# Kernel optimization log

Hardware: AMD Instinct MI355X
Metric: run time of the kernel (lower is better)

## Reference

```python
import jax, jax.numpy as jnp
import numpy as np


def setup_inputs() -> dict:
    key = jax.random.key(0)
    k_x, k_m, k_w1, k_b1, k_w2, k_b2 = jax.random.split(key, 6)
    b, seq_len, d_in, d_out = 8, 4096, 1024, 512
    x = jax.random.normal(k_x, (b, seq_len, d_in), dtype=jnp.float32)
    # binary-ish mask in {0,1} as floats (torch code multiplies by mask)
    mask = (jax.random.uniform(k_m, (b, seq_len)) < 0.5).astype(jnp.float32)
    s1 = 1.0 / np.sqrt(d_in)
    s2 = 1.0 / np.sqrt(d_out)
    W_enc = jax.random.uniform(k_w1, (d_out, d_in), minval=-s1, maxval=s1, dtype=jnp.float32)
    b_enc = jax.random.uniform(k_b1, (d_out,), minval=-s1, maxval=s1, dtype=jnp.float32)
    W_dec = jax.random.uniform(k_w2, (d_in, d_out), minval=-s2, maxval=s2, dtype=jnp.float32)
    b_dec = jax.random.uniform(k_b2, (d_in,), minval=-s2, maxval=s2, dtype=jnp.float32)
    return {"x": x, "mask": mask, "W_enc": W_enc, "b_enc": b_enc, "W_dec": W_dec, "b_dec": b_dec}


def reference(x, mask, W_enc, b_enc, W_dec, b_dec):
    # per-step: v_t = v_{t-1} + relu(x_t @ W_enc^T + b_enc) * mask_t  -> additive scan == cumsum
    h = jax.nn.relu(jnp.einsum('bsd,od->bso', x, W_enc) + b_enc) * mask[:, :, None]  # [b,s,d_out]
    v_cum = jnp.cumsum(h, axis=1)  # [b,s,d_out]
    out_enc = jnp.einsum('bso,do->bsd', v_cum, W_dec) + b_dec  # decode every prefix state
    v = v_cum[:, -1, :]  # final accumulated state
    return (v, out_enc)
```

## Files before the change

kernel.cpp:

```cpp
#include <hip/hip_runtime.h>
#include <hip/hip_bf16.h>
#include <stdint.h>

typedef __bf16 bf16_t;
typedef __bf16 bf16x4 __attribute__((ext_vector_type(4)));
typedef __bf16 bf16x8 __attribute__((ext_vector_type(8)));
typedef float  f32x4  __attribute__((ext_vector_type(4)));

__device__ __forceinline__ void gload_lds16(const void* g, void* l) {
  __builtin_amdgcn_global_load_lds(
      (__attribute__((address_space(1))) void*)g,
      (__attribute__((address_space(3))) void*)l, 16, 0, 0);
}

__global__ void cast_weights(const float* __restrict__ a, bf16_t* __restrict__ oa,
                             const float* __restrict__ b, bf16_t* __restrict__ ob,
                             int n4each) {
  const int i = blockIdx.x * blockDim.x + threadIdx.x;
  const float* src; bf16_t* dst; int k;
  if (i < n4each) { src = a; dst = oa; k = i; }
  else            { src = b; dst = ob; k = i - n4each; }
  f32x4 v = reinterpret_cast<const f32x4*>(src)[k];
  bf16x4 o;
  o[0] = (bf16_t)v[0]; o[1] = (bf16_t)v[1]; o[2] = (bf16_t)v[2]; o[3] = (bf16_t)v[3];
  reinterpret_cast<bf16x4*>(dst)[k] = o;
}

#define PHASE_SYNC() do { \
  __builtin_amdgcn_s_barrier(); \
  asm volatile("s_waitcnt lgkmcnt(0)" ::: "memory"); \
  __builtin_amdgcn_sched_barrier(0); \
  __builtin_amdgcn_s_setprio(1); \
} while (0)

#define PHASE_END() do { \
  __builtin_amdgcn_s_setprio(0); \
  __builtin_amdgcn_s_barrier(); \
} while (0)

#define QUAD(RH, CH, BF) do { \
  _Pragma("unroll") \
  for (int fr = 0; fr < 4; ++fr) { \
    _Pragma("unroll") \
    for (int fc = 0; fc < 2; ++fc) { \
      acc[RH][CH][fr][fc] = __builtin_amdgcn_mfma_f32_16x16x32_bf16(a[fr][0], BF[fc][0], acc[RH][CH][fr][fc], 0, 0, 0); \
      acc[RH][CH][fr][fc] = __builtin_amdgcn_mfma_f32_16x16x32_bf16(a[fr][1], BF[fc][1], acc[RH][CH][fr][fc], 0, 0, 0); \
    } \
  } \
} while (0)

__global__ __launch_bounds__(512, 2) void gemm1_f8p(
    const float* __restrict__ x, const bf16_t* __restrict__ Wenc,
    const float* __restrict__ b_enc, const float* __restrict__ mask,
    bf16_t* __restrict__ h_out, float* __restrict__ partials)
{
  __shared__ __align__(16) char smem[131072];
  auto Al = [&](int buf) { return (bf16_t*)(smem + buf * 32768); };
  auto Bl = [&](int buf) { return (bf16_t*)(smem + 65536 + buf * 32768); };

  const int tid  = threadIdx.x;
  const int lane = tid & 63;
  const int w    = tid >> 6;
  const int wm   = w >> 2;
  const int wn   = w & 3;
  const long bm  = (long)blockIdx.x * 256;
  const long bn  = (long)blockIdx.y * 256;
  const int NT   = 16;

  f32x4  acc[2][2][4][2] = {};
  bf16x8 a[4][2], b0[2][2], b1[2][2];
  f32x4  av[8];

  const int scolB = (((lane & 7) ^ (lane >> 3)) << 3);
  auto stageB = [&](int t, int h) {
    bf16_t* lb = Bl(t & 1);
    #pragma unroll
    for (int c = 0; c < 2; ++c) {
      const int r0 = h * 128 + (w * 2 + c) * 8;
      gload_lds16(Wenc + (bn + r0 + (lane >> 3)) * 1024 + t * 64 + scolB, lb + r0 * 64);
    }
  };
  auto gaLoad = [&](int t) {
    #pragma unroll
    for (int u = 0; u < 8; ++u) {
      const int row = u * 32 + (tid >> 4);
      av[u] = *reinterpret_cast<const f32x4*>(x + (bm + row) * 1024 + t * 64 + (tid & 15) * 4);
    }
  };
  auto aWrite = [&](int t) {
    bf16_t* lb = Al(t & 1);
    const int c4 = tid & 15;
    #pragma unroll
    for (int u = 0; u < 8; ++u) {
      const int row = u * 32 + (tid >> 4);
      bf16x4 o;
      o[0] = (bf16_t)av[u][0]; o[1] = (bf16_t)av[u][1];
      o[2] = (bf16_t)av[u][2]; o[3] = (bf16_t)av[u][3];
      *reinterpret_cast<bf16x4*>(lb + row * 64 + ((((c4 >> 1) ^ (row & 7)) << 3) + (c4 & 1) * 4)) = o;
    }
  };

  const int fcb0 = ((((lane >> 4)    ) ^ (lane & 7)) << 3);
  const int fcb1 = ((((lane >> 4) + 4) ^ (lane & 7)) << 3);
  auto loadA = [&](int buf, int rh) {
    const bf16_t* lb = Al(buf);
    #pragma unroll
    for (int fr = 0; fr < 4; ++fr) {
      const int row = rh * 128 + wm * 64 + fr * 16 + (lane & 15);
      a[fr][0] = *reinterpret_cast<const bf16x8*>(lb + row * 64 + fcb0);
      a[fr][1] = *reinterpret_cast<const bf16x8*>(lb + row * 64 + fcb1);
    }
  };
  auto loadB = [&](int buf, int ch, bf16x8 (&bf)[2][2]) {
    const bf16_t* lb = Bl(buf);
    #pragma unroll
    for (int fc = 0; fc < 2; ++fc) {
      const int row = ch * 128 + wn * 32 + fc * 16 + (lane & 15);
      bf[fc][0] = *reinterpret_cast<const bf16x8*>(lb + row * 64 + fcb0);
      bf[fc][1] = *reinterpret_cast<const bf16x8*>(lb + row * 64 + fcb1);
    }
  };

  __builtin_amdgcn_sched_barrier(0);
  stageB(0, 0); stageB(0, 1);
  gaLoad(0);
  stageB(1, 0); stageB(1, 1);
  aWrite(0);
  asm volatile("s_waitcnt lgkmcnt(0)" ::: "memory");
  __builtin_amdgcn_s_barrier();

  for (int t = 0; t < NT; ++t) {
    const int buf = t & 1;
    const bool g1 = (t + 1 < NT);
    const bool g2 = (t + 2 < NT);

    if (g1) gaLoad(t + 1);
    loadA(buf, 0); loadB(buf, 0, b0);
    PHASE_SYNC(); QUAD(0, 0, b0); PHASE_END();

    loadB(buf, 1, b1);
    if (g2) stageB(t + 2, 0);
    PHASE_SYNC(); QUAD(0, 1, b1); PHASE_END();

    loadA(buf, 1);
    if (g2) stageB(t + 2, 1);
    PHASE_SYNC(); QUAD(1, 0, b0); PHASE_END();

    if (g1) aWrite(t + 1);
    PHASE_SYNC(); QUAD(1, 1, b1);
    __builtin_amdgcn_s_setprio(0);
    asm volatile("s_waitcnt vmcnt(4)" ::: "memory");
    __builtin_amdgcn_s_barrier();
  }
  asm volatile("s_waitcnt vmcnt(0) lgkmcnt(0)" ::: "memory");
  __builtin_amdgcn_s_barrier();
  __builtin_amdgcn_sched_barrier(0);

  bf16_t* tile = (bf16_t*)smem;
  float bv[2][2];
  #pragma unroll
  for (int ch = 0; ch < 2; ++ch)
    #pragma unroll
    for (int fc = 0; fc < 2; ++fc)
      bv[ch][fc] = b_enc[bn + ch * 128 + wn * 32 + fc * 16 + (lane & 15)];

  #pragma unroll
  for (int rh = 0; rh < 2; ++rh)
    #pragma unroll
    for (int fr = 0; fr < 4; ++fr) {
      const int row0 = rh * 128 + wm * 64 + fr * 16 + ((lane >> 4) << 2);
      const f32x4 mv = *reinterpret_cast<const f32x4*>(&mask[bm + row0]);
      #pragma unroll
      for (int ch = 0; ch < 2; ++ch)
        #pragma unroll
        for (int fc = 0; fc < 2; ++fc) {
          const int col = ch * 128 + wn * 32 + fc * 16 + (lane & 15);
          #pragma unroll
          for (int e = 0; e < 4; ++e) {
            const int row = row0 + e;
            float hv = acc[rh][ch][fr][fc][e] + bv[ch][fc];
            hv = (hv > 0.f ? hv : 0.f) * mv[e];
            tile[row * 256 + (col ^ (((row >> 2) & 3) << 4))] = (bf16_t)hv;
          }
        }
    }
  __syncthreads();

  const int sub = tid >> 8;
  const int col = tid & 255;
  float run = 0.f;
  bf16_t* hp = h_out + (bm + sub * 128) * 512 + bn + col;
  #pragma unroll 4
  for (int s = 0; s < 128; ++s) {
    const int row = sub * 128 + s;
    run += (float)tile[row * 256 + (col ^ (((row >> 2) & 3) << 4))];
    hp[(long)s * 512] = (bf16_t)run;
  }
  partials[(blockIdx.x * 2 + sub) * 512 + bn + col] = run;
}

__global__ __launch_bounds__(512, 2) void gemm2_8p(
    const bf16_t* __restrict__ A, const bf16_t* __restrict__ B,
    const int K, const int N,
    const float* __restrict__ Padd,
    float* __restrict__ outf)
{
  __shared__ __align__(16) char smem[131072];

  const int tid  = threadIdx.x;
  const int lane = tid & 63;
  const int w    = tid >> 6;
  const int wm   = w >> 2;
  const int wn   = w & 3;
  const long bm  = (long)blockIdx.x * 256;
  const long bn  = (long)blockIdx.y * 256;
  const int NT   = K >> 6;

  const int scol = (((lane & 7) ^ (lane >> 3)) << 3);
  const int fcb0 = ((((lane >> 4)    ) ^ (lane & 7)) << 3);
  const int fcb1 = ((((lane >> 4) + 4) ^ (lane & 7)) << 3);

  f32x4  acc[2][2][4][2] = {};
  bf16x8 a[4][2], b0[2][2], b1[2][2];

  auto Albs = [&](int buf) { return (bf16_t*)(smem + buf * 65536); };
  auto Blbs = [&](int buf) { return (bf16_t*)(smem + buf * 65536 + 32768); };

  auto stageA = [&](int t, int h) {
    bf16_t* lb = Albs(t & 1);
    #pragma unroll
    for (int c = 0; c < 2; ++c) {
      const int r0 = h * 128 + (w * 2 + c) * 8;
      gload_lds16(A + (bm + r0 + (lane >> 3)) * (long)K + t * 64 + scol, lb + r0 * 64);
    }
  };
  auto stageB = [&](int t, int h) {
    bf16_t* lb = Blbs(t & 1);
    #pragma unroll
    for (int c = 0; c < 2; ++c) {
      const int r0 = h * 128 + (w * 2 + c) * 8;
      gload_lds16(B + (bn + r0 + (lane >> 3)) * (long)K + t * 64 + scol, lb + r0 * 64);
    }
  };
  auto loadA = [&](int buf, int rh) {
    const bf16_t* lb = Albs(buf);
    #pragma unroll
    for (int fr = 0; fr < 4; ++fr) {
      const int row = rh * 128 + wm * 64 + fr * 16 + (lane & 15);
      a[fr][0] = *reinterpret_cast<const bf16x8*>(lb + row * 64 + fcb0);
      a[fr][1] = *reinterpret_cast<const bf16x8*>(lb + row * 64 + fcb1);
    }
  };
  auto loadB = [&](int buf, int ch, bf16x8 (&bf)[2][2]) {
    const bf16_t* lb = Blbs(buf);
    #pragma unroll
    for (int fc = 0; fc < 2; ++fc) {
      const int row = ch * 128 + wn * 32 + fc * 16 + (lane & 15);
      bf[fc][0] = *reinterpret_cast<const bf16x8*>(lb + row * 64 + fcb0);
      bf[fc][1] = *reinterpret_cast<const bf16x8*>(lb + row * 64 + fcb1);
    }
  };

  __builtin_amdgcn_sched_barrier(0);
  stageA(0, 0); stageA(0, 1); stageB(0, 0); stageB(0, 1);
  stageA(1, 0); stageA(1, 1); stageB(1, 0); stageB(1, 1);
  asm volatile("s_waitcnt vmcnt(8)" ::: "memory");
  __builtin_amdgcn_s_barrier();

  for (int t = 0; t < NT; ++t) {
    const int buf = t & 1;
    const bool g2 = (t + 2 < NT);

    loadA(buf, 0); loadB(buf, 0, b0);
    PHASE_SYNC(); QUAD(0, 0, b0); PHASE_END();

    loadB(buf, 1, b1);
    if (g2) stageA(t + 2, 0);
    PHASE_SYNC(); QUAD(0, 1, b1); PHASE_END();

    loadA(buf, 1);
    if (g2) stageB(t + 2, 0);
    PHASE_SYNC(); QUAD(1, 0, b0); PHASE_END();

    if (g2) { stageA(t + 2, 1); stageB(t + 2, 1); }
    PHASE_SYNC(); QUAD(1, 1, b1);
    __builtin_amdgcn_s_setprio(0);
    if (g2) asm volatile("s_waitcnt vmcnt(8)" ::: "memory");
    else    asm volatile("s_waitcnt vmcnt(0)" ::: "memory");
    __builtin_amdgcn_s_barrier();
  }
  __builtin_amdgcn_sched_barrier(0);

  #pragma unroll
  for (int rh = 0; rh < 2; ++rh)
    #pragma unroll
    for (int ch = 0; ch < 2; ++ch)
      #pragma unroll
      for (int fc = 0; fc < 2; ++fc) {
        const long gc = bn + ch * 128 + wn * 32 + fc * 16 + (lane & 15);
        const float pv = Padd[(blockIdx.x * 2 + rh) * (long)N + gc];
        #pragma unroll
        for (int fr = 0; fr < 4; ++fr) {
          const long gr = bm + rh * 128 + wm * 64 + fr * 16 + ((lane >> 4) << 2);
          #pragma unroll
          for (int e = 0; e < 4; ++e)
            outf[(gr + e) * (long)N + gc] = acc[rh][ch][fr][fc][e] + pv;
        }
      }
}

__global__ __launch_bounds__(256) void gemm_p(
    const bf16_t* __restrict__ A, const bf16_t* __restrict__ B,
    const int K, const int N,
    const float* __restrict__ bias,
    float* __restrict__ outf)
{
  __shared__ __align__(16) bf16_t As[2][128 * 64];
  __shared__ __align__(16) bf16_t Bs[2][128 * 64];

  const int tid  = threadIdx.x;
  const int lane = tid & 63;
  const int w    = tid >> 6;
  const int wm   = w >> 1, wn = w & 1;
  const long bm  = (long)blockIdx.x * 128;
  const long bn  = (long)blockIdx.y * 128;

  f32x4 acc[4][4] = {};

  const int srow = w * 32 + (lane >> 3);
  const int scol = (lane & 7) * 8;
  const bf16_t* Abase = A + (bm + srow) * (long)K + scol;
  const bf16_t* Bbase = B + (bn + srow) * (long)K + scol;

  auto stage = [&](bf16_t* da, bf16_t* db, int kt) {
    #pragma unroll
    for (int it = 0; it < 4; ++it) {
      gload_lds16(Abase + (long)it * 8 * K + kt, &da[(w * 32 + it * 8) * 64]);
      gload_lds16(Bbase + (long)it * 8 * K + kt, &db[(w * 32 + it * 8) * 64]);
    }
  };
  auto mfma_tile = [&](const bf16_t* Asb, const bf16_t* Bsb) {
    #pragma unroll
    for (int kk = 0; kk < 2; ++kk) {
      const int kof = kk * 32 + (lane >> 4) * 8;
      bf16x8 afr[4], bfr[4];
      #pragma unroll
      for (int i = 0; i < 4; ++i)
        afr[i] = *reinterpret_cast<const bf16x8*>(&Asb[(wm * 64 + i * 16 + (lane & 15)) * 64 + kof]);
      #pragma unroll
      for (int j = 0; j < 4; ++j)
        bfr[j] = *reinterpret_cast<const bf16x8*>(&Bsb[(wn * 64 + j * 16 + (lane & 15)) * 64 + kof]);
      #pragma unroll
      for (int i = 0; i < 4; ++i)
        #pragma unroll
        for (int j = 0; j < 4; ++j)
          acc[i][j] = __builtin_amdgcn_mfma_f32_16x16x32_bf16(afr[i], bfr[j], acc[i][j], 0, 0, 0);
    }
  };

  stage(As[0], Bs[0], 0);
  __syncthreads();
  int kt = 64;
  for (int p2 = 0; p2 < (K >> 7); ++p2) {
    if (kt < K) stage(As[1], Bs[1], kt);
    mfma_tile(As[0], Bs[0]);
    __syncthreads();
    kt += 64;
    if (kt < K) stage(As[0], Bs[0], kt);
    mfma_tile(As[1], Bs[1]);
    __syncthreads();
    kt += 64;
  }

  #pragma unroll
  for (int j = 0; j < 4; ++j) {
    const long gc = bn + wn * 64 + j * 16 + (lane & 15);
    const float addv = bias[gc];
    #pragma unroll
    for (int i = 0; i < 4; ++i) {
      const long gr0 = bm + wm * 64 + i * 16 + ((lane >> 4) << 2);
      #pragma unroll
      for (int r = 0; r < 4; ++r)
        outf[(gr0 + r) * (long)N + gc] = acc[i][j][r] + addv;
    }
  }
}

__global__ void scan_chunks(const float* __restrict__ partials, bf16_t* __restrict__ prefixb,
                            float* __restrict__ v_out) {
  const int idx = blockIdx.x * blockDim.x + threadIdx.x;
  const int b = idx >> 9;
  const int o = idx & 511;
  float run = 0.f;
  #pragma unroll
  for (int c = 0; c < 32; ++c) {
    const size_t off = ((size_t)(b * 32 + c)) * 512 + o;
    prefixb[off] = (bf16_t)run;
    run += partials[off];
  }
  v_out[idx] = run;
}

extern "C" void kernel_launch(void* const* d_in, const int* in_sizes, int n_in,
                              void* d_out, int out_size, void* d_ws, size_t ws_size,
                              hipStream_t stream) {
  const float* x     = (const float*)d_in[0];
  const float* mask  = (const float*)d_in[1];
  const float* W_enc = (const float*)d_in[2];
  const float* b_enc = (const float*)d_in[3];
  const float* W_dec = (const float*)d_in[4];
  const float* b_dec = (const float*)d_in[5];

  float* out     = (float*)d_out;
  float* v_out   = out;
  float* out_enc = out + 4096;

  char* ws = (char*)d_ws;
  bf16_t* Web      = (bf16_t*)ws;  ws += (size_t)512 * 1024 * 2;
  bf16_t* Wdb      = (bf16_t*)ws;  ws += (size_t)1024 * 512 * 2;
  bf16_t* h        = (bf16_t*)ws;  ws += (size_t)32768 * 512 * 2;
  float*  partials = (float*)ws;   ws += (size_t)256 * 512 * 4;
  bf16_t* prefixb  = (bf16_t*)ws;  ws += (size_t)256 * 512 * 2;
  float*  P        = (float*)ws;   ws += (size_t)256 * 1024 * 4;

  cast_weights<<<1024, 256, 0, stream>>>(W_enc, Web, W_dec, Wdb, 131072);

  gemm1_f8p<<<dim3(128, 2), 512, 0, stream>>>(x, Web, b_enc, mask, h, partials);

  scan_chunks<<<16, 256, 0, stream>>>(partials, prefixb, v_out);

  gemm_p<<<dim3(2, 8), 256, 0, stream>>>(prefixb, Wdb, 512, 1024, b_dec, P);

  gemm2_8p<<<dim3(128, 4), 512, 0, stream>>>(h, Wdb, 512, 1024, P, out_enc);
}
```

Before: 142.7 us.

## Fuse chunk prefix scan and prefix-decode GEMM into gemm2 prologue

Removes the scan_chunks and gemm_p launches. Each gemm2 block now computes its own chunk prefix sums from partials, writes the final state v, and computes the prefix-times-W_dec correction for its 256 columns with a scalar dot product into LDS. This saves two kernel launches and the P/prefixb round trips through global memory. In exchange, every block does redundant serial prefix and 512-long dot-product work before its main MFMA loop, which adds latency to each block.

```diff
diff --git a/kernel.cpp b/kernel.cpp
--- a/kernel.cpp
+++ b/kernel.cpp
@@ -199,13 +199,13 @@
   partials[(blockIdx.x * 2 + sub) * 512 + bn + col] = run;
 }
 
-__global__ __launch_bounds__(512, 2) void gemm2_8p(
+__global__ __launch_bounds__(512, 2) void gemm2_fused(
     const bf16_t* __restrict__ A, const bf16_t* __restrict__ B,
-    const int K, const int N,
-    const float* __restrict__ Padd,
-    float* __restrict__ outf)
+    const float* __restrict__ partials, const float* __restrict__ b_dec,
+    float* __restrict__ v_out, float* __restrict__ outf)
 {
   __shared__ __align__(16) char smem[131072];
+  __shared__ __align__(16) float Plds[2][256];
 
   const int tid  = threadIdx.x;
   const int lane = tid & 63;
@@ -214,7 +214,43 @@
   const int wn   = w & 3;
   const long bm  = (long)blockIdx.x * 256;
   const long bn  = (long)blockIdx.y * 256;
-  const int NT   = K >> 6;
+  const int  K = 512, N = 1024, NT = 8;
+
+  {
+    float* pref = (float*)smem;
+    const int bx  = blockIdx.x;
+    const int b   = bx >> 4;
+    const int cc0 = (bx & 15) * 2;
+    const int o   = tid;
+    float s = 0.f;
+    for (int k = 0; k < cc0; ++k)
+      s += partials[((size_t)(b * 32 + k)) * 512 + o];
+    const float pc0 = partials[((size_t)bx * 2) * 512 + o];
+    pref[o]       = s;
+    pref[512 + o] = s + pc0;
+    if ((bx & 15) == 15 && blockIdx.y == 0)
+      v_out[(size_t)b * 512 + o] = s + pc0 + partials[((size_t)bx * 2 + 1) * 512 + o];
+    __syncthreads();
+
+    const int c  = tid >> 8;
+    const int gi = tid & 255;
+    const long gc = bn + gi;
+    const float* pr = pref + c * 512;
+    const bf16_t* wr = B + gc * (long)K;
+    float pacc = b_dec[gc];
+    for (int oo = 0; oo < 512; oo += 8) {
+      const bf16x8 wv = *reinterpret_cast<const bf16x8*>(wr + oo);
+      const f32x4 p0 = *reinterpret_cast<const f32x4*>(pr + oo);
+      const f32x4 p1 = *reinterpret_cast<const f32x4*>(pr + oo + 4);
+      #pragma unroll
+      for (int e = 0; e < 4; ++e) {
+        pacc += p0[e] * (float)wv[e];
+        pacc += p1[e] * (float)wv[e + 4];
+      }
+    }
+    Plds[c][gi] = pacc;
+    __syncthreads();
+  }
 
   const int scol = (((lane & 7) ^ (lane >> 3)) << 3);
   const int fcb0 = ((((lane >> 4)    ) ^ (lane & 7)) << 3);
@@ -297,8 +333,9 @@
     for (int ch = 0; ch < 2; ++ch)
       #pragma unroll
       for (int fc = 0; fc < 2; ++fc) {
-        const long gc = bn + ch * 128 + wn * 32 + fc * 16 + (lane & 15);
-        const float pv = Padd[(blockIdx.x * 2 + rh) * (long)N + gc];
+        const int  gi = ch * 128 + wn * 32 + fc * 16 + (lane & 15);
+        const long gc = bn + gi;
+        const float pv = Plds[rh][gi];
         #pragma unroll
         for (int fr = 0; fr < 4; ++fr) {
           const long gr = bm + rh * 128 + wm * 64 + fr * 16 + ((lane >> 4) << 2);
@@ -307,98 +344,6 @@
             outf[(gr + e) * (long)N + gc] = acc[rh][ch][fr][fc][e] + pv;
         }
       }
-}
-
-__global__ __launch_bounds__(256) void gemm_p(
-    const bf16_t* __restrict__ A, const bf16_t* __restrict__ B,
-    const int K, const int N,
-    const float* __restrict__ bias,
-    float* __restrict__ outf)
-{
-  __shared__ __align__(16) bf16_t As[2][128 * 64];
-  __shared__ __align__(16) bf16_t Bs[2][128 * 64];
-
-  const int tid  = threadIdx.x;
-  const int lane = tid & 63;
-  const int w    = tid >> 6;
-  const int wm   = w >> 1, wn = w & 1;
-  const long bm  = (long)blockIdx.x * 128;
-  const long bn  = (long)blockIdx.y * 128;
-
-  f32x4 acc[4][4] = {};
-
-  const int srow = w * 32 + (lane >> 3);
-  const int scol = (lane & 7) * 8;
-  const bf16_t* Abase = A + (bm + srow) * (long)K + scol;
-  const bf16_t* Bbase = B + (bn + srow) * (long)K + scol;
-
-  auto stage = [&](bf16_t* da, bf16_t* db, int kt) {
-    #pragma unroll
-    for (int it = 0; it < 4; ++it) {
-      gload_lds16(Abase + (long)it * 8 * K + kt, &da[(w * 32 + it * 8) * 64]);
-      gload_lds16(Bbase + (long)it * 8 * K + kt, &db[(w * 32 + it * 8) * 64]);
-    }
-  };
-  auto mfma_tile = [&](const bf16_t* Asb, const bf16_t* Bsb) {
-    #pragma unroll
-    for (int kk = 0; kk < 2; ++kk) {
-      const int kof = kk * 32 + (lane >> 4) * 8;
-      bf16x8 afr[4], bfr[4];
-      #pragma unroll
-      for (int i = 0; i < 4; ++i)
-        afr[i] = *reinterpret_cast<const bf16x8*>(&Asb[(wm * 64 + i * 16 + (lane & 15)) * 64 + kof]);
-      #pragma unroll
-      for (int j = 0; j < 4; ++j)
-        bfr[j] = *reinterpret_cast<const bf16x8*>(&Bsb[(wn * 64 + j * 16 + (lane & 15)) * 64 + kof]);
-      #pragma unroll
-      for (int i = 0; i < 4; ++i)
-        #pragma unroll
-        for (int j = 0; j < 4; ++j)
-          acc[i][j] = __builtin_amdgcn_mfma_f32_16x16x32_bf16(afr[i], bfr[j], acc[i][j], 0, 0, 0);
-    }
-  };
-
-  stage(As[0], Bs[0], 0);
-  __syncthreads();
-  int kt = 64;
-  for (int p2 = 0; p2 < (K >> 7); ++p2) {
-    if (kt < K) stage(As[1], Bs[1], kt);
-    mfma_tile(As[0], Bs[0]);
-    __syncthreads();
-    kt += 64;
-    if (kt < K) stage(As[0], Bs[0], kt);
-    mfma_tile(As[1], Bs[1]);
-    __syncthreads();
-    kt += 64;
-  }
-
-  #pragma unroll
-  for (int j = 0; j < 4; ++j) {
-    const long gc = bn + wn * 64 + j * 16 + (lane & 15);
-    const float addv = bias[gc];
-    #pragma unroll
-    for (int i = 0; i < 4; ++i) {
-      const long gr0 = bm + wm * 64 + i * 16 + ((lane >> 4) << 2);
-      #pragma unroll
-      for (int r = 0; r < 4; ++r)
-        outf[(gr0 + r) * (long)N + gc] = acc[i][j][r] + addv;
-    }
-  }
-}
-
-__global__ void scan_chunks(const float* __restrict__ partials, bf16_t* __restrict__ prefixb,
-                            float* __restrict__ v_out) {
-  const int idx = blockIdx.x * blockDim.x + threadIdx.x;
-  const int b = idx >> 9;
-  const int o = idx & 511;
-  float run = 0.f;
-  #pragma unroll
-  for (int c = 0; c < 32; ++c) {
-    const size_t off = ((size_t)(b * 32 + c)) * 512 + o;
-    prefixb[off] = (bf16_t)run;
-    run += partials[off];
-  }
-  v_out[idx] = run;
 }
 
 extern "C" void kernel_launch(void* const* d_in, const int* in_sizes, int n_in,
@@ -420,16 +365,10 @@
   bf16_t* Wdb      = (bf16_t*)ws;  ws += (size_t)1024 * 512 * 2;
   bf16_t* h        = (bf16_t*)ws;  ws += (size_t)32768 * 512 * 2;
   float*  partials = (float*)ws;   ws += (size_t)256 * 512 * 4;
-  bf16_t* prefixb  = (bf16_t*)ws;  ws += (size_t)256 * 512 * 2;
-  float*  P        = (float*)ws;   ws += (size_t)256 * 1024 * 4;
 
   cast_weights<<<1024, 256, 0, stream>>>(W_enc, Web, W_dec, Wdb, 131072);
 
   gemm1_f8p<<<dim3(128, 2), 512, 0, stream>>>(x, Web, b_enc, mask, h, partials);
 
-  scan_chunks<<<16, 256, 0, stream>>>(partials, prefixb, v_out);
-
-  gemm_p<<<dim3(2, 8), 256, 0, stream>>>(prefixb, Wdb, 512, 1024, b_dec, P);
-
-  gemm2_8p<<<dim3(128, 4), 512, 0, stream>>>(h, Wdb, 512, 1024, P, out_enc);
-}
+  gemm2_fused<<<dim3(128, 4), 512, 0, stream>>>(h, Wdb, partials, b_dec, v_out, out_enc);
+}
```

Result: slower. 158.3 us (+11.0%).
